# Kernel optimization log

Measured on AMD Instinct MI355X. Metric: run time of the kernel, lower is better.

## Reference

```python
import jax, jax.numpy as jnp
import numpy as np
from jax import lax

ALPHA = 0.3  # SSGConv alpha


def _cdist(x):
    # Euclidean distance matrix [N, N] for x: [N, H]
    n2 = jnp.sum(x * x, axis=-1)
    d2 = n2[:, None] + n2[None, :] - 2.0 * (x @ x.T)
    return jnp.sqrt(jnp.maximum(d2, 0.0))


def _prim(dist):
    # Dense O(N^2) Prim MST starting at node 0. Returns (parents, children, weights), each [N-1].
    N = dist.shape[0]
    INF = jnp.float32(1e30)
    in_tree = jnp.zeros(N, dtype=bool).at[0].set(True)
    mind = dist[0]                       # best edge weight into tree per node
    parent = jnp.zeros(N, dtype=jnp.int32)

    def step(carry, _):
        in_tree, mind, parent = carry
        d = jnp.where(in_tree, INF, mind)
        v = jnp.argmin(d).astype(jnp.int32)
        w = d[v]
        p = parent[v]
        in_tree = in_tree.at[v].set(True)
        newd = dist[v]
        upd = newd < mind
        mind = jnp.where(upd, newd, mind)
        parent = jnp.where(upd, v, parent)
        return (in_tree, mind, parent), (p, v, w)

    _, (ps, vs, ws) = lax.scan(step, (in_tree, mind, parent), None, length=N - 1)
    return ps, vs, ws


def _build_edges(features):
    # Torch code detaches edge weights via .item(); mirror with stop_gradient.
    B, N, _ = features.shape
    dist = jax.vmap(_cdist)(lax.stop_gradient(features))   # [B, N, N]
    ps, vs, ws = jax.vmap(_prim)(dist)                     # each [B, N-1]
    off = (jnp.arange(B, dtype=jnp.int32) * N)[:, None]
    a = (ps + off).ravel()
    b = (vs + off).ravel()
    src = jnp.concatenate([a, b])   # MST edges are added in both directions
    dst = jnp.concatenate([b, a])
    ew = jnp.concatenate([ws.ravel(), ws.ravel()])
    return src, dst, ew


def _gcn_norm(src, dst, ew, num_nodes):
    # PyG gcn_norm: add self loops (weight 1), symmetric deg^-1/2 normalization.
    loop = jnp.arange(num_nodes, dtype=src.dtype)
    src = jnp.concatenate([src, loop])
    dst = jnp.concatenate([dst, loop])
    ew = jnp.concatenate([ew, jnp.ones(num_nodes, ew.dtype)])
    deg = jax.ops.segment_sum(ew, dst, num_segments=num_nodes)
    dinv = jnp.where(deg > 0, lax.rsqrt(jnp.maximum(deg, 1e-30)), 0.0)
    norm = dinv[src] * ew * dinv[dst]
    return src, dst, norm


def _ssg_conv(x, src, dst, norm, W, b, num_nodes):
    # SSGConv with K=1: h = alpha*x + (1-alpha)*A_hat x, then linear.
    prop = jax.ops.segment_sum(norm[:, None] * x[src], dst, num_segments=num_nodes)
    h = ALPHA * x + (1.0 - ALPHA) * prop
    return h @ W + b


def _forward(features, W1, b1, W2, b2, W3, b3, Wd, bd, Wo, bo):
    B, N, H = features.shape
    NT = B * N
    src, dst, ew = _build_edges(features)
    src, dst, norm = _gcn_norm(src, dst, ew, NT)
    x = features.reshape(NT, H)
    x = jnp.tanh(_ssg_conv(x, src, dst, norm, W1, b1, NT))
    x = jnp.tanh(_ssg_conv(x, src, dst, norm, W2, b2, NT))
    x = jnp.tanh(_ssg_conv(x, src, dst, norm, W3, b3, NT))
    # dropout: eval mode -> identity. global_mean_pool: each graph has exactly N nodes.
    pooled = x.reshape(B, N, -1).mean(axis=1)          # [B, 2H]
    h = jnp.tanh(pooled @ Wd + bd)                     # [B, H]
    return h @ Wo + bo                                 # [B, num_labels]


def setup_inputs() -> dict:
    key = jax.random.key(0)
    ks = jax.random.split(key, 12)
    B, N, H, L = 16, 1024, 256, 8
    H2 = 2 * H

    def lin(k, fin, fout):
        s = 1.0 / np.sqrt(fin)
        k1, k2 = jax.random.split(k)
        return (jax.random.uniform(k1, (fin, fout), jnp.float32, -s, s),
                jax.random.uniform(k2, (fout,), jnp.float32, -s, s))

    W1, b1 = lin(ks[1], H, H2)
    W2, b2 = lin(ks[2], H2, H2)
    W3, b3 = lin(ks[3], H2, H2)
    Wd, bd = lin(ks[4], H2, H)
    Wo, bo = lin(ks[5], H, L)
    features = jax.random.normal(ks[0], (B, N, H), jnp.float32)
    return {"features": features, "W1": W1, "b1": b1, "W2": W2, "b2": b2,
            "W3": W3, "b3": b3, "Wd": Wd, "bd": bd, "Wo": Wo, "bo": bo}


def reference(features, W1, b1, W2, b2, W3, b3, Wd, bd, Wo, bo):
    return _forward(features, W1, b1, W2, b2, W3, b3, Wd, bd, Wo, bo)
```

## Files before the change

kernel.cpp:

```cpp
#include <hip/hip_runtime.h>
#include <math.h>

namespace {

constexpr float ALPHA = 0.3f;
constexpr int B  = 16;
constexpr int N  = 1024;
constexpr int H  = 256;
constexpr int H2 = 512;
constexpr int NT = B * N;
constexpr int NE = N - 1;
constexpr int CAP = 32;

__device__ __forceinline__ unsigned umin32(unsigned a, unsigned b) { return a < b ? a : b; }

__global__ void n2_kernel(const float* __restrict__ x, float* __restrict__ n2) {
  int wave = threadIdx.x >> 6, lane = threadIdx.x & 63;
  int row  = blockIdx.x * 4 + wave;
  float4 v = *(const float4*)(x + (size_t)row * H + lane * 4);
  float s  = v.x * v.x + v.y * v.y + v.z * v.z + v.w * v.w;
  #pragma unroll
  for (int off = 32; off; off >>= 1) s += __shfl_xor(s, off);
  if (lane == 0) n2[row] = s;
}

__global__ __launch_bounds__(256) void dist_kernel(const float* __restrict__ x,
    const float* __restrict__ n2, float* __restrict__ dist) {
  __shared__ float As[16][132], Bs[16][132];
  const int bb = blockIdx.z;
  int idx = blockIdx.x, ti = 0;
  while (idx >= 8 - ti) { idx -= 8 - ti; ++ti; }
  const int tj = ti + idx;
  const int i0 = ti * 128, j0 = tj * 128;
  const int t = threadIdx.x, tx = t & 15, ty = t >> 4;
  const float* xb = x + (size_t)bb * N * H;
  float acc[8][8] = {};
  for (int kc = 0; kc < H; kc += 16) {
    #pragma unroll
    for (int u = 0; u < 2; ++u) {
      int q = t + u * 256;
      int row = q >> 2, kf = (q & 3) * 4;
      float4 a = *(const float4*)(xb + (size_t)(i0 + row) * H + kc + kf);
      As[kf + 0][row] = a.x; As[kf + 1][row] = a.y;
      As[kf + 2][row] = a.z; As[kf + 3][row] = a.w;
      float4 bv = *(const float4*)(xb + (size_t)(j0 + row) * H + kc + kf);
      Bs[kf + 0][row] = bv.x; Bs[kf + 1][row] = bv.y;
      Bs[kf + 2][row] = bv.z; Bs[kf + 3][row] = bv.w;
    }
    __syncthreads();
    #pragma unroll
    for (int kk = 0; kk < 16; ++kk) {
      float4 a0 = *(const float4*)&As[kk][ty * 4];
      float4 a1 = *(const float4*)&As[kk][64 + ty * 4];
      float4 b0 = *(const float4*)&Bs[kk][tx * 4];
      float4 b1 = *(const float4*)&Bs[kk][64 + tx * 4];
      float ar[8] = {a0.x,a0.y,a0.z,a0.w,a1.x,a1.y,a1.z,a1.w};
      float br[8] = {b0.x,b0.y,b0.z,b0.w,b1.x,b1.y,b1.z,b1.w};
      #pragma unroll
      for (int r = 0; r < 8; ++r)
        #pragma unroll
        for (int c = 0; c < 8; ++c) acc[r][c] += ar[r] * br[c];
    }
    __syncthreads();
  }
  float n2i[8], n2j[8];
  #pragma unroll
  for (int r = 0; r < 8; ++r)
    n2i[r] = n2[bb * N + i0 + (r < 4 ? ty * 4 + r : 64 + ty * 4 + r - 4)];
  #pragma unroll
  for (int c = 0; c < 8; ++c)
    n2j[c] = n2[bb * N + j0 + (c < 4 ? tx * 4 + c : 64 + tx * 4 + c - 4)];
  const bool mirror = (ti != tj);
  float* distb = dist + (size_t)bb * N * N;
  #pragma unroll
  for (int r = 0; r < 8; ++r) {
    int mi = i0 + (r < 4 ? ty * 4 + r : 64 + ty * 4 + r - 4);
    float o[8];
    #pragma unroll
    for (int c = 0; c < 8; ++c) {
      float d2 = (n2i[r] + n2j[c]) - 2.0f * acc[r][c];
      o[c] = sqrtf(fmaxf(d2, 0.0f));
    }
    float* dst = distb + (size_t)mi * N + j0;
    *(float4*)(dst + tx * 4)      = make_float4(o[0], o[1], o[2], o[3]);
    *(float4*)(dst + 64 + tx * 4) = make_float4(o[4], o[5], o[6], o[7]);
    if (mirror) {
      #pragma unroll
      for (int c = 0; c < 8; ++c) {
        int mj = j0 + (c < 4 ? tx * 4 + c : 64 + tx * 4 + c - 4);
        distb[(size_t)mj * N + mi] = o[c];
      }
    }
  }
}

__device__ __forceinline__ unsigned wave_min_u32(unsigned x) {
  unsigned t;
  t = (unsigned)__builtin_amdgcn_update_dpp((int)x, (int)x, 0x111, 0xf, 0xf, false); x = umin32(x, t);
  t = (unsigned)__builtin_amdgcn_update_dpp((int)x, (int)x, 0x112, 0xf, 0xf, false); x = umin32(x, t);
  t = (unsigned)__builtin_amdgcn_update_dpp((int)x, (int)x, 0x114, 0xf, 0xf, false); x = umin32(x, t);
  t = (unsigned)__builtin_amdgcn_update_dpp((int)x, (int)x, 0x118, 0xf, 0xf, false); x = umin32(x, t);
  x = umin32(x, (unsigned)__shfl_xor((int)x, 16));
  x = umin32(x, (unsigned)__shfl_xor((int)x, 32));
  return (unsigned)__builtin_amdgcn_readlane((int)x, 63);
}

struct Sel2 { unsigned w; int j; };

__device__ __forceinline__ Sel2 block_select(unsigned mw0, unsigned mw1,
    unsigned mw2, unsigned mw3, int wid, int lane, unsigned long long* smin) {
  unsigned lm = umin32(umin32(mw0, mw1), umin32(mw2, mw3));
  unsigned wm = wave_min_u32(lm);
  unsigned mb = (mw0 == wm ? 1u : 0u) | (mw1 == wm ? 2u : 0u) |
                (mw2 == wm ? 4u : 0u) | (mw3 == wm ? 8u : 0u);
  unsigned long long bal = __ballot(mb != 0);
  int fl = __ffsll(bal) - 1;
  int slot = __ffs((unsigned)__builtin_amdgcn_readlane((int)mb, fl)) - 1;
  int widx = (wid << 8) | (fl << 2) | slot;
  if (lane == 0)
    smin[wid] = ((unsigned long long)wm << 32) | (unsigned)widx;
  __syncthreads();
  unsigned long long k0 = smin[0], k1 = smin[1], k2 = smin[2], k3 = smin[3];
  unsigned long long ka = k0 < k1 ? k0 : k1;
  unsigned long long kb = k2 < k3 ? k2 : k3;
  unsigned long long kk = ka < kb ? ka : kb;
  __syncthreads();
  Sel2 r; r.w = (unsigned)(kk >> 32); r.j = (int)(unsigned)(kk & 0xFFFFFFFFu);
  return r;
}

__global__ __launch_bounds__(256) void prim_gemm1_kernel(
    const float* __restrict__ dist, const float* __restrict__ feat,
    const float* __restrict__ W1, int* __restrict__ ep, int* __restrict__ ev,
    float* __restrict__ ewt, float* __restrict__ y) {
  __shared__ unsigned long long smin[4];
  __shared__ int epv[NE];
  __shared__ int evv[NE];
  __shared__ float ews[NE];
  __shared__ float As[16][132], Bs[16][132];
  if (blockIdx.x < B) {
    const int b = blockIdx.x;
    const int tid = threadIdx.x, wid = tid >> 6, lane = tid & 63;
    const float* Db = dist + (size_t)b * N * N;
    const int jbase = tid * 4;

    unsigned d0, d1, d2, d3;
    {
      float4 v = *(const float4*)(Db + jbase);
      d0 = __float_as_uint(v.x); d1 = __float_as_uint(v.y);
      d2 = __float_as_uint(v.z); d3 = __float_as_uint(v.w);
    }
    unsigned mw0 = d0, mw1 = d1, mw2 = d2, mw3 = d3;
    unsigned rm0 = 0, rm1 = 0, rm2 = 0, rm3 = 0;
    int pa0 = 0, pa1 = 0, pa2 = 0, pa3 = 0;
    if (tid == 0) { rm0 = ~0u; mw0 = ~0u; }

    Sel2 s0 = block_select(mw0, mw1, mw2, mw3, wid, lane, smin);
    int cj = s0.j;
    if ((cj >> 2) == tid) {
      int sl = cj & 3;
      int pv = pa0; if (sl == 1) pv = pa1; if (sl == 2) pv = pa2; if (sl == 3) pv = pa3;
      epv[0] = pv; evv[0] = cj; ews[0] = __uint_as_float(s0.w);
      if (sl == 0) { rm0 = ~0u; mw0 = ~0u; }
      if (sl == 1) { rm1 = ~0u; mw1 = ~0u; }
      if (sl == 2) { rm2 = ~0u; mw2 = ~0u; }
      if (sl == 3) { rm3 = ~0u; mw3 = ~0u; }
    }
    float4 xq = *(const float4*)(Db + (size_t)cj * N + jbase);

    for (int k = 1; k < NE; ++k) {
      unsigned r0 = __float_as_uint(xq.x), r1 = __float_as_uint(xq.y);
      unsigned r2 = __float_as_uint(xq.z), r3 = __float_as_uint(xq.w);
      unsigned q0 = r0 | rm0, q1 = r1 | rm1, q2 = r2 | rm2, q3 = r3 | rm3;
      mw0 = umin32(mw0, q0); mw1 = umin32(mw1, q1);
      mw2 = umin32(mw2, q2); mw3 = umin32(mw3, q3);
      Sel2 se = block_select(mw0, mw1, mw2, mw3, wid, lane, smin);
      const int nj = se.j;
      float4 nxt = *(const float4*)(Db + (size_t)nj * N + jbase);
      if (r0 < d0) { pa0 = cj; d0 = r0; }
      if (r1 < d1) { pa1 = cj; d1 = r1; }
      if (r2 < d2) { pa2 = cj; d2 = r2; }
      if (r3 < d3) { pa3 = cj; d3 = r3; }
      if ((nj >> 2) == tid) {
        int sl = nj & 3;
        int pv = pa0; if (sl == 1) pv = pa1; if (sl == 2) pv = pa2; if (sl == 3) pv = pa3;
        epv[k] = pv; evv[k] = nj; ews[k] = __uint_as_float(se.w);
        if (sl == 0) { rm0 = ~0u; mw0 = ~0u; }
        if (sl == 1) { rm1 = ~0u; mw1 = ~0u; }
        if (sl == 2) { rm2 = ~0u; mw2 = ~0u; }
        if (sl == 3) { rm3 = ~0u; mw3 = ~0u; }
      }
      cj = nj; xq = nxt;
    }

    __syncthreads();
    for (int e = tid; e < NE; e += 256) {
      ep[b * NE + e]  = epv[e];
      ev[b * NE + e]  = evv[e];
      ewt[b * NE + e] = ews[e];
    }
  } else {
    const int gb = blockIdx.x - B;
    const int m0 = (gb >> 2) * 128, n0 = (gb & 3) * 128;
    const int t = threadIdx.x, tx = t & 15, ty = t >> 4;
    float acc[8][8] = {};
    for (int kc = 0; kc < H; kc += 16) {
      #pragma unroll
      for (int u = 0; u < 2; ++u) {
        int q = t + u * 256;
        int row = q >> 2, kf = (q & 3) * 4;
        float4 a = *(const float4*)(feat + (size_t)(m0 + row) * H + kc + kf);
        As[kf + 0][row] = a.x; As[kf + 1][row] = a.y;
        As[kf + 2][row] = a.z; As[kf + 3][row] = a.w;
        int rowB = q >> 5, cf = (q & 31) * 4;
        *(float4*)&Bs[rowB][cf] = *(const float4*)(W1 + (size_t)(kc + rowB) * H2 + n0 + cf);
      }
      __syncthreads();
      #pragma unroll
      for (int kk = 0; kk < 16; ++kk) {
        float4 a0 = *(const float4*)&As[kk][ty * 4];
        float4 a1 = *(const float4*)&As[kk][64 + ty * 4];
        float4 b0 = *(const float4*)&Bs[kk][tx * 4];
        float4 b1 = *(const float4*)&Bs[kk][64 + tx * 4];
        float ar[8] = {a0.x,a0.y,a0.z,a0.w,a1.x,a1.y,a1.z,a1.w};
        float br[8] = {b0.x,b0.y,b0.z,b0.w,b1.x,b1.y,b1.z,b1.w};
        #pragma unroll
        for (int r = 0; r < 8; ++r)
          #pragma unroll
          for (int c = 0; c < 8; ++c) acc[r][c] += ar[r] * br[c];
      }
      __syncthreads();
    }
    #pragma unroll
    for (int r = 0; r < 8; ++r) {
      int m = m0 + (r < 4 ? ty * 4 + r : 64 + ty * 4 + r - 4);
      float* dst = y + (size_t)m * H2 + n0;
      *(float4*)(dst + tx * 4)      = make_float4(acc[r][0], acc[r][1], acc[r][2], acc[r][3]);
      *(float4*)(dst + 64 + tx * 4) = make_float4(acc[r][4], acc[r][5], acc[r][6], acc[r][7]);
    }
  }
}

__global__ void adj_kernel(const int* __restrict__ ep, const int* __restrict__ ev,
    const float* __restrict__ ewt, int* __restrict__ adjI, float* __restrict__ adjW,
    int* __restrict__ cnt, float* __restrict__ dinv) {
  int i = blockIdx.x * 256 + threadIdx.x;
  int b = i >> 10, loc = i & 1023;
  const int* epb = ep + b * NE;
  const int* evb = ev + b * NE;
  const float* ewb = ewt + b * NE;
  int c = 0; float wsum = 0.0f;
  for (int k = 0; k < NE; ++k) {
    int p = epb[k], v = evb[k];
    if (p == loc || v == loc) {
      float w = ewb[k];
      wsum += w;
      int nb = (p == loc) ? v : p;
      if (c < CAP) { adjI[i * CAP + c] = (b << 10) + nb; adjW[i * CAP + c] = w; }
      ++c;
    }
  }
  cnt[i]  = c < CAP ? c : CAP;
  dinv[i] = 1.0f / sqrtf(wsum + 1.0f);
}

__global__ void finish1_kernel(const float* __restrict__ y, const int* __restrict__ adjI,
    const float* __restrict__ adjW, const int* __restrict__ cnt,
    const float* __restrict__ dinv, const float* __restrict__ b1,
    float* __restrict__ out1) {
  int wave = threadIdx.x >> 6, lane = threadIdx.x & 63;
  int i = blockIdx.x * 4 + wave;
  float dv = dinv[i];
  int c = cnt[i];
  float selfc = ALPHA + (1.0f - ALPHA) * dv * dv;
  float4 acc[2];
  const float* yi = y + (size_t)i * H2 + lane * 4;
  #pragma unroll
  for (int u = 0; u < 2; ++u) {
    float4 v = *(const float4*)(yi + u * 256);
    acc[u].x = selfc * v.x; acc[u].y = selfc * v.y;
    acc[u].z = selfc * v.z; acc[u].w = selfc * v.w;
  }
  for (int e = 0; e < c; ++e) {
    int j   = adjI[i * CAP + e];
    float w = adjW[i * CAP + e];
    float coef = (1.0f - ALPHA) * dv * (w * dinv[j]);
    const float* yj = y + (size_t)j * H2 + lane * 4;
    #pragma unroll
    for (int u = 0; u < 2; ++u) {
      float4 v = *(const float4*)(yj + u * 256);
      acc[u].x += coef * v.x; acc[u].y += coef * v.y;
      acc[u].z += coef * v.z; acc[u].w += coef * v.w;
    }
  }
  float* ho = out1 + (size_t)i * H2 + lane * 4;
  #pragma unroll
  for (int u = 0; u < 2; ++u) {
    float4 bb = *(const float4*)(b1 + lane * 4 + u * 256);
    float4 o;
    o.x = tanhf(acc[u].x + bb.x); o.y = tanhf(acc[u].y + bb.y);
    o.z = tanhf(acc[u].z + bb.z); o.w = tanhf(acc[u].w + bb.w);
    *(float4*)(ho + u * 256) = o;
  }
}

template <int HH>
__global__ void prop_kernel(const float* __restrict__ x, const int* __restrict__ adjI,
    const float* __restrict__ adjW, const int* __restrict__ cnt,
    const float* __restrict__ dinv, float* __restrict__ h) {
  constexpr int U = HH / 256;
  int wave = threadIdx.x >> 6, lane = threadIdx.x & 63;
  int i = blockIdx.x * 4 + wave;
  float dv = dinv[i];
  int c = cnt[i];
  float selfc = ALPHA + (1.0f - ALPHA) * dv * dv;
  float4 acc[U];
  const float* xi = x + (size_t)i * HH + lane * 4;
  #pragma unroll
  for (int u = 0; u < U; ++u) {
    float4 v = *(const float4*)(xi + u * 256);
    acc[u].x = selfc * v.x; acc[u].y = selfc * v.y;
    acc[u].z = selfc * v.z; acc[u].w = selfc * v.w;
  }
  for (int e = 0; e < c; ++e) {
    int j   = adjI[i * CAP + e];
    float w = adjW[i * CAP + e];
    float coef = (1.0f - ALPHA) * dv * (w * dinv[j]);
    const float* xj = x + (size_t)j * HH + lane * 4;
    #pragma unroll
    for (int u = 0; u < U; ++u) {
      float4 v = *(const float4*)(xj + u * 256);
      acc[u].x += coef * v.x; acc[u].y += coef * v.y;
      acc[u].z += coef * v.z; acc[u].w += coef * v.w;
    }
  }
  float* ho = h + (size_t)i * HH + lane * 4;
  #pragma unroll
  for (int u = 0; u < U; ++u) *(float4*)(ho + u * 256) = acc[u];
}

template <int K>
__global__ __launch_bounds__(256) void gemm_tanh_kernel(const float* __restrict__ A,
    const float* __restrict__ W, const float* __restrict__ bias, float* __restrict__ C) {
  __shared__ float As[16][132], Bs[16][132];
  const int m0 = blockIdx.x * 128, n0 = blockIdx.y * 128;
  const int t = threadIdx.x, tx = t & 15, ty = t >> 4;
  float acc[8][8] = {};
  for (int kc = 0; kc < K; kc += 16) {
    #pragma unroll
    for (int u = 0; u < 2; ++u) {
      int q = t + u * 256;
      int row = q >> 2, kf = (q & 3) * 4;
      float4 a = *(const float4*)(A + (size_t)(m0 + row) * K + kc + kf);
      As[kf + 0][row] = a.x; As[kf + 1][row] = a.y;
      As[kf + 2][row] = a.z; As[kf + 3][row] = a.w;
      int rowB = q >> 5, cf = (q & 31) * 4;
      *(float4*)&Bs[rowB][cf] = *(const float4*)(W + (size_t)(kc + rowB) * H2 + n0 + cf);
    }
    __syncthreads();
    #pragma unroll
    for (int kk = 0; kk < 16; ++kk) {
      float4 a0 = *(const float4*)&As[kk][ty * 4];
      float4 a1 = *(const float4*)&As[kk][64 + ty * 4];
      float4 b0 = *(const float4*)&Bs[kk][tx * 4];
      float4 b1 = *(const float4*)&Bs[kk][64 + tx * 4];
      float ar[8] = {a0.x,a0.y,a0.z,a0.w,a1.x,a1.y,a1.z,a1.w};
      float br[8] = {b0.x,b0.y,b0.z,b0.w,b1.x,b1.y,b1.z,b1.w};
      #pragma unroll
      for (int r = 0; r < 8; ++r)
        #pragma unroll
        for (int c = 0; c < 8; ++c) acc[r][c] += ar[r] * br[c];
    }
    __syncthreads();
  }
  float4 bi0 = *(const float4*)(bias + n0 + tx * 4);
  float4 bi1 = *(const float4*)(bias + n0 + 64 + tx * 4);
  float bb[8] = {bi0.x,bi0.y,bi0.z,bi0.w,bi1.x,bi1.y,bi1.z,bi1.w};
  #pragma unroll
  for (int r = 0; r < 8; ++r) {
    int m = m0 + (r < 4 ? ty * 4 + r : 64 + ty * 4 + r - 4);
    float o[8];
    #pragma unroll
    for (int c = 0; c < 8; ++c) o[c] = tanhf(acc[r][c] + bb[c]);
    float* dst = C + (size_t)m * H2 + n0;
    *(float4*)(dst + tx * 4)      = make_float4(o[0], o[1], o[2], o[3]);
    *(float4*)(dst + 64 + tx * 4) = make_float4(o[4], o[5], o[6], o[7]);
  }
}

__global__ void pool_kernel(const float* __restrict__ x, float* __restrict__ pooled) {
  int b = blockIdx.x;
  int c = blockIdx.y * 256 + threadIdx.x;
  const float* xb = x + ((size_t)b << 10) * H2 + c;
  float s = 0.0f;
  for (int i = 0; i < N; ++i) s += xb[(size_t)i * H2];
  pooled[b * H2 + c] = s * (1.0f / N);
}

__global__ void head_kernel(const float* __restrict__ pooled, const float* __restrict__ Wd,
    const float* __restrict__ bd, const float* __restrict__ Wo, const float* __restrict__ bo,
    float* __restrict__ out) {
  __shared__ float sp[512], sh[256];
  int b = blockIdx.x, t = threadIdx.x;
  sp[t] = pooled[b * H2 + t];
  sp[t + 256] = pooled[b * H2 + t + 256];
  __syncthreads();
  float acc = bd[t];
  for (int c2 = 0; c2 < 512; ++c2) acc += sp[c2] * Wd[c2 * 256 + t];
  sh[t] = tanhf(acc);
  __syncthreads();
  if (t < 8) {
    float o = bo[t];
    for (int j = 0; j < 256; ++j) o += sh[j] * Wo[j * 8 + t];
    out[b * 8 + t] = o;
  }
}

}

extern "C" void kernel_launch(void* const* d_in, const int* in_sizes, int n_in,
                              void* d_out, int out_size, void* d_ws, size_t ws_size,
                              hipStream_t stream) {
  const float* feat = (const float*)d_in[0];
  const float* W1 = (const float*)d_in[1];
  const float* b1 = (const float*)d_in[2];
  const float* W2 = (const float*)d_in[3];
  const float* b2 = (const float*)d_in[4];
  const float* W3 = (const float*)d_in[5];
  const float* b3 = (const float*)d_in[6];
  const float* Wd = (const float*)d_in[7];
  const float* bd = (const float*)d_in[8];
  const float* Wo = (const float*)d_in[9];
  const float* bo = (const float*)d_in[10];
  float* out = (float*)d_out;
  char* ws = (char*)d_ws;

  float* dist = (float*)(ws);
  float* out1 = (float*)(ws);
  float* x2   = (float*)(ws + ((size_t)32 << 20));
  float* x3   = (float*)(ws);
  float* ybuf = (float*)(ws + ((size_t)64 << 20));
  float* hbuf = (float*)(ws + ((size_t)64 << 20));
  char* misc  = ws + ((size_t)96 << 20);
  int*   ep     = (int*)(misc);
  int*   ev     = (int*)(misc + 65536);
  float* ewt    = (float*)(misc + 131072);
  int*   cnt    = (int*)(misc + 196608);
  float* dinv   = (float*)(misc + 262144);
  int*   adjI   = (int*)(misc + 327680);
  float* adjW   = (float*)(misc + 327680 + 2097152);
  float* n2     = (float*)(misc + 327680 + 2 * 2097152);
  float* pooled = (float*)(misc + 327680 + 2 * 2097152 + 65536);

  n2_kernel<<<NT / 4, 256, 0, stream>>>(feat, n2);
  dist_kernel<<<dim3(36, 1, 16), 256, 0, stream>>>(feat, n2, dist);
  prim_gemm1_kernel<<<B + (NT / 128) * 4, 256, 0, stream>>>(
      dist, feat, W1, ep, ev, ewt, ybuf);
  adj_kernel<<<NT / 256, 256, 0, stream>>>(ep, ev, ewt, adjI, adjW, cnt, dinv);

  finish1_kernel<<<NT / 4, 256, 0, stream>>>(ybuf, adjI, adjW, cnt, dinv, b1, out1);
  prop_kernel<512><<<NT / 4, 256, 0, stream>>>(out1, adjI, adjW, cnt, dinv, hbuf);
  gemm_tanh_kernel<512><<<dim3(NT / 128, 4), 256, 0, stream>>>(hbuf, W2, b2, x2);
  prop_kernel<512><<<NT / 4, 256, 0, stream>>>(x2, adjI, adjW, cnt, dinv, hbuf);
  gemm_tanh_kernel<512><<<dim3(NT / 128, 4), 256, 0, stream>>>(hbuf, W3, b3, x3);

  pool_kernel<<<dim3(B, H2 / 256), 256, 0, stream>>>(x3, pooled);
  head_kernel<<<B, 256, 0, stream>>>(pooled, Wd, bd, Wo, bo, out);
}
```

Before: 1.228 ms.

## Use split-bf16 MFMA matrix cores for the two dense tanh GEMMs

Replaces the scalar FP32 tiled GEMM used for the second and third SSG layers with an MFMA kernel. Each FP32 operand is split into high and low bf16 halves, and three 16x16x32 bf16 MFMAs per tile (hi*hi, lo*hi, hi*lo) approximate FP32 accuracy. The aim is to move the 16384x512x512 GEMMs from vector ALUs onto matrix cores. The cost is per-tile conversion work, a transposed scalar LDS store for W, uncoalesced scalar output stores, and a small loss of precision from dropping the lo*lo term.

```diff
diff --git a/kernel.cpp b/kernel.cpp
--- a/kernel.cpp
+++ b/kernel.cpp
@@ -13,6 +13,9 @@
 constexpr int CAP = 32;
 
 __device__ __forceinline__ unsigned umin32(unsigned a, unsigned b) { return a < b ? a : b; }
+
+typedef __attribute__((ext_vector_type(8))) short short8;
+typedef __attribute__((ext_vector_type(4))) float f32x4;
 
 __global__ void n2_kernel(const float* __restrict__ x, float* __restrict__ n2) {
   int wave = threadIdx.x >> 6, lane = threadIdx.x & 63;
@@ -339,52 +342,99 @@
   for (int u = 0; u < U; ++u) *(float4*)(ho + u * 256) = acc[u];
 }
 
-template <int K>
-__global__ __launch_bounds__(256) void gemm_tanh_kernel(const float* __restrict__ A,
+__device__ __forceinline__ void bf16split(float a, unsigned short& hi, unsigned short& lo) {
+  unsigned u = __float_as_uint(a);
+  hi = (unsigned short)(u >> 16);
+  float fh = __uint_as_float(u & 0xFFFF0000u);
+  float fl = a - fh;
+  lo = (unsigned short)(__float_as_uint(fl) >> 16);
+}
+
+__global__ __launch_bounds__(256) void mgemm_tanh_kernel(const float* __restrict__ A,
     const float* __restrict__ W, const float* __restrict__ bias, float* __restrict__ C) {
-  __shared__ float As[16][132], Bs[16][132];
+  __shared__ unsigned short Ahi[128][40], Alo[128][40];
+  __shared__ unsigned short Bhi[128][40], Blo[128][40];
   const int m0 = blockIdx.x * 128, n0 = blockIdx.y * 128;
-  const int t = threadIdx.x, tx = t & 15, ty = t >> 4;
-  float acc[8][8] = {};
-  for (int kc = 0; kc < K; kc += 16) {
-    #pragma unroll
-    for (int u = 0; u < 2; ++u) {
-      int q = t + u * 256;
-      int row = q >> 2, kf = (q & 3) * 4;
-      float4 a = *(const float4*)(A + (size_t)(m0 + row) * K + kc + kf);
-      As[kf + 0][row] = a.x; As[kf + 1][row] = a.y;
-      As[kf + 2][row] = a.z; As[kf + 3][row] = a.w;
-      int rowB = q >> 5, cf = (q & 31) * 4;
-      *(float4*)&Bs[rowB][cf] = *(const float4*)(W + (size_t)(kc + rowB) * H2 + n0 + cf);
+  const int t = threadIdx.x;
+  const int w = t >> 6, lane = t & 63;
+  const int lrow = lane & 15, lk = (lane >> 4) * 8;
+  f32x4 acc[2][8];
+  #pragma unroll
+  for (int mt = 0; mt < 2; ++mt)
+    #pragma unroll
+    for (int nt = 0; nt < 8; ++nt) acc[mt][nt] = (f32x4){0.f, 0.f, 0.f, 0.f};
+
+  const int arow = t >> 1, akq = (t & 1) * 16;
+  const int wr = t & 31, wc4 = (t >> 5) * 16;
+
+  for (int kc = 0; kc < H2; kc += 32) {
+    {
+      const float* src = A + (size_t)(m0 + arow) * H2 + kc + akq;
+      unsigned short h[16], l[16];
+      #pragma unroll
+      for (int i = 0; i < 16; i += 4) {
+        float4 v = *(const float4*)(src + i);
+        bf16split(v.x, h[i], l[i]);     bf16split(v.y, h[i+1], l[i+1]);
+        bf16split(v.z, h[i+2], l[i+2]); bf16split(v.w, h[i+3], l[i+3]);
+      }
+      short8 ph0 = {(short)h[0],(short)h[1],(short)h[2],(short)h[3],
+                    (short)h[4],(short)h[5],(short)h[6],(short)h[7]};
+      short8 ph1 = {(short)h[8],(short)h[9],(short)h[10],(short)h[11],
+                    (short)h[12],(short)h[13],(short)h[14],(short)h[15]};
+      short8 pl0 = {(short)l[0],(short)l[1],(short)l[2],(short)l[3],
+                    (short)l[4],(short)l[5],(short)l[6],(short)l[7]};
+      short8 pl1 = {(short)l[8],(short)l[9],(short)l[10],(short)l[11],
+                    (short)l[12],(short)l[13],(short)l[14],(short)l[15]};
+      *(short8*)&Ahi[arow][akq]     = ph0;
+      *(short8*)&Ahi[arow][akq + 8] = ph1;
+      *(short8*)&Alo[arow][akq]     = pl0;
+      *(short8*)&Alo[arow][akq + 8] = pl1;
+    }
+    {
+      const float* wsrc = W + (size_t)(kc + wr) * H2 + n0 + wc4;
+      #pragma unroll
+      for (int i = 0; i < 16; i += 4) {
+        float4 v = *(const float4*)(wsrc + i);
+        unsigned short h0,h1,h2,h3,l0,l1,l2,l3;
+        bf16split(v.x, h0, l0); bf16split(v.y, h1, l1);
+        bf16split(v.z, h2, l2); bf16split(v.w, h3, l3);
+        Bhi[wc4+i+0][wr] = h0; Bhi[wc4+i+1][wr] = h1;
+        Bhi[wc4+i+2][wr] = h2; Bhi[wc4+i+3][wr] = h3;
+        Blo[wc4+i+0][wr] = l0; Blo[wc4+i+1][wr] = l1;
+        Blo[wc4+i+2][wr] = l2; Blo[wc4+i+3][wr] = l3;
+      }
     }
     __syncthreads();
-    #pragma unroll
-    for (int kk = 0; kk < 16; ++kk) {
-      float4 a0 = *(const float4*)&As[kk][ty * 4];
-      float4 a1 = *(const float4*)&As[kk][64 + ty * 4];
-      float4 b0 = *(const float4*)&Bs[kk][tx * 4];
-      float4 b1 = *(const float4*)&Bs[kk][64 + tx * 4];
-      float ar[8] = {a0.x,a0.y,a0.z,a0.w,a1.x,a1.y,a1.z,a1.w};
-      float br[8] = {b0.x,b0.y,b0.z,b0.w,b1.x,b1.y,b1.z,b1.w};
-      #pragma unroll
-      for (int r = 0; r < 8; ++r)
-        #pragma unroll
-        for (int c = 0; c < 8; ++c) acc[r][c] += ar[r] * br[c];
+    const int r0 = w * 32 + lrow;
+    short8 a0h = *(const short8*)&Ahi[r0][lk];
+    short8 a0l = *(const short8*)&Alo[r0][lk];
+    short8 a1h = *(const short8*)&Ahi[r0 + 16][lk];
+    short8 a1l = *(const short8*)&Alo[r0 + 16][lk];
+    #pragma unroll
+    for (int nt = 0; nt < 8; ++nt) {
+      short8 bh = *(const short8*)&Bhi[nt * 16 + lrow][lk];
+      short8 bl = *(const short8*)&Blo[nt * 16 + lrow][lk];
+      acc[0][nt] = __builtin_amdgcn_mfma_f32_16x16x32_bf16(a0h, bh, acc[0][nt], 0, 0, 0);
+      acc[0][nt] = __builtin_amdgcn_mfma_f32_16x16x32_bf16(a0l, bh, acc[0][nt], 0, 0, 0);
+      acc[0][nt] = __builtin_amdgcn_mfma_f32_16x16x32_bf16(a0h, bl, acc[0][nt], 0, 0, 0);
+      acc[1][nt] = __builtin_amdgcn_mfma_f32_16x16x32_bf16(a1h, bh, acc[1][nt], 0, 0, 0);
+      acc[1][nt] = __builtin_amdgcn_mfma_f32_16x16x32_bf16(a1l, bh, acc[1][nt], 0, 0, 0);
+      acc[1][nt] = __builtin_amdgcn_mfma_f32_16x16x32_bf16(a1h, bl, acc[1][nt], 0, 0, 0);
     }
     __syncthreads();
   }
-  float4 bi0 = *(const float4*)(bias + n0 + tx * 4);
-  float4 bi1 = *(const float4*)(bias + n0 + 64 + tx * 4);
-  float bb[8] = {bi0.x,bi0.y,bi0.z,bi0.w,bi1.x,bi1.y,bi1.z,bi1.w};
-  #pragma unroll
-  for (int r = 0; r < 8; ++r) {
-    int m = m0 + (r < 4 ? ty * 4 + r : 64 + ty * 4 + r - 4);
-    float o[8];
-    #pragma unroll
-    for (int c = 0; c < 8; ++c) o[c] = tanhf(acc[r][c] + bb[c]);
-    float* dst = C + (size_t)m * H2 + n0;
-    *(float4*)(dst + tx * 4)      = make_float4(o[0], o[1], o[2], o[3]);
-    *(float4*)(dst + 64 + tx * 4) = make_float4(o[4], o[5], o[6], o[7]);
+  #pragma unroll
+  for (int mt = 0; mt < 2; ++mt) {
+    #pragma unroll
+    for (int nt = 0; nt < 8; ++nt) {
+      int col = n0 + nt * 16 + lrow;
+      float bcol = bias[col];
+      #pragma unroll
+      for (int i = 0; i < 4; ++i) {
+        int row = m0 + w * 32 + mt * 16 + (lane >> 4) * 4 + i;
+        C[(size_t)row * H2 + col] = tanhf(acc[mt][nt][i] + bcol);
+      }
+    }
   }
 }
 
@@ -460,9 +510,9 @@
 
   finish1_kernel<<<NT / 4, 256, 0, stream>>>(ybuf, adjI, adjW, cnt, dinv, b1, out1);
   prop_kernel<512><<<NT / 4, 256, 0, stream>>>(out1, adjI, adjW, cnt, dinv, hbuf);
-  gemm_tanh_kernel<512><<<dim3(NT / 128, 4), 256, 0, stream>>>(hbuf, W2, b2, x2);
+  mgemm_tanh_kernel<<<dim3(NT / 128, 4), 256, 0, stream>>>(hbuf, W2, b2, x2);
   prop_kernel<512><<<NT / 4, 256, 0, stream>>>(x2, adjI, adjW, cnt, dinv, hbuf);
-  gemm_tanh_kernel<512><<<dim3(NT / 128, 4), 256, 0, stream>>>(hbuf, W3, b3, x3);
+  mgemm_tanh_kernel<<<dim3(NT / 128, 4), 256, 0, stream>>>(hbuf, W3, b3, x3);
 
   pool_kernel<<<dim3(B, H2 / 256), 256, 0, stream>>>(x3, pooled);
   head_kernel<<<B, 256, 0, stream>>>(pooled, Wd, bd, Wo, bo, out);
```

Measured after the change: 1.093 ms. 11.1% less time.
